# Kernel tuning notes

Hardware: AMD Instinct MI355X
Metric: run time of the kernel (lower is better)

Reference implementation:

```python
import jax, jax.numpy as jnp
import numpy as np

DIM = 1024
HEADS = 16

def setup_inputs() -> dict:
    key = jax.random.key(0)
    k1, k2 = jax.random.split(key)
    x = jax.random.normal(k1, (4, 2048, DIM), dtype=jnp.float32)
    # torch nn.Linear(dim, 3*dim, bias=False): weight shape [3*dim, dim], y = x @ W.T
    W_qkv = jax.random.normal(k2, (3 * DIM, DIM), dtype=jnp.float32) * (DIM ** -0.5)
    return {"x": x, "W_qkv": W_qkv}

def reference(x, W_qkv):
    B, N, D = x.shape
    H = HEADS
    hd = D // H
    scale = hd ** -0.5
    qkv = jnp.einsum('bnd,ed->bne', x, W_qkv)            # [B,N,3D]
    qkv = qkv.reshape(B, N, 3, H, hd).transpose(2, 0, 3, 1, 4)  # [3,B,H,N,hd]
    q, k, v = qkv[0], qkv[1], qkv[2]
    attn = jnp.einsum('bhnd,bhmd->bhnm', q, k) * scale   # [B,H,N,N]
    attn = jax.nn.softmax(attn, axis=-1)                 # dropout is identity at eval
    out = jnp.einsum('bhnm,bhmd->bhnd', attn, v)         # [B,H,N,hd]
    return out.transpose(0, 2, 1, 3).reshape(B, N, D)
```

## Files before the change

kernel.cpp:

```cpp
#include <hip/hip_runtime.h>

typedef unsigned short ushort_t;
typedef short bf16x8 __attribute__((ext_vector_type(8)));
typedef float f32x4 __attribute__((ext_vector_type(4)));
typedef float f32x16 __attribute__((ext_vector_type(16)));

__device__ __forceinline__ unsigned f2bf(float f) {
  union { float f; unsigned u; } v; v.f = f;
  return (v.u + 0x7FFFu + ((v.u >> 16) & 1u)) >> 16;
}

__device__ __forceinline__ void gll16(const void* g, const void* l) {
  __builtin_amdgcn_global_load_lds(
      (const __attribute__((address_space(1))) void*)g,
      (__attribute__((address_space(3))) void*)l, 16, 0, 0);
}

__global__ __launch_bounds__(256) void cvt_both(const float* __restrict__ x,
                                                const float* __restrict__ W,
                                                ushort_t* __restrict__ xb,
                                                ushort_t* __restrict__ wb) {
  int bid = blockIdx.x;
  const float* src;
  ushort_t* dst;
  int i;
  if (bid < 8192) { src = x; dst = xb; i = bid * 256 + threadIdx.x; }
  else            { src = W; dst = wb; i = (bid - 8192) * 256 + threadIdx.x; }
  float4 v = ((const float4*)src)[i];
  uint2 o;
  o.x = f2bf(v.x) | (f2bf(v.y) << 16);
  o.y = f2bf(v.z) | (f2bf(v.w) << 16);
  ((uint2*)dst)[i] = o;
}

__global__ __launch_bounds__(256) void gemm_qkv(const ushort_t* __restrict__ A,
                                                const ushort_t* __restrict__ Bw,
                                                ushort_t* __restrict__ qk,
                                                ushort_t* __restrict__ VT) {
  __shared__ ushort_t As[128 * 64];
  __shared__ ushort_t Bs[128 * 64];
  const int tid = threadIdx.x;
  const int w = tid >> 6, ln = tid & 63;
  const int g = ln >> 4, lr = ln & 15;
  const int bx = blockIdx.x;
  const int swz = (bx & 7) * 192 + (bx >> 3);
  const int nt = swz % 24, mt = swz / 24;
  const int m0 = mt * 128, n0 = nt * 128;
  const int wr = w >> 1, wc = w & 1;
  const float cscale = (nt < 8) ? 0.18033688f : 1.0f;

  f32x4 acc[4][4] = {};

  for (int kt = 0; kt < 16; ++kt) {
#pragma unroll
    for (int q = 0; q < 4; ++q) {
      int chunk = w * 256 + q * 64 + ln;
      int r = chunk >> 3, c = chunk & 7;
      int cs = c ^ (r & 7);
      gll16(A + (size_t)(m0 + r) * 1024 + kt * 64 + cs * 8, As + chunk * 8);
      gll16(Bw + (size_t)(n0 + r) * 1024 + kt * 64 + cs * 8, Bs + chunk * 8);
    }
    __syncthreads();
#pragma unroll
    for (int ks = 0; ks < 2; ++ks) {
      bf16x8 af[4], bfr[4];
#pragma unroll
      for (int mi = 0; mi < 4; ++mi) {
        int row = wr * 64 + mi * 16 + lr;
        af[mi] = *(const bf16x8*)((const char*)As + row * 128 +
                                  ((g * 16 + ks * 64) ^ ((row & 7) << 4)));
      }
#pragma unroll
      for (int ni = 0; ni < 4; ++ni) {
        int row = wc * 64 + ni * 16 + lr;
        bfr[ni] = *(const bf16x8*)((const char*)Bs + row * 128 +
                                   ((g * 16 + ks * 64) ^ ((row & 7) << 4)));
      }
#pragma unroll
      for (int mi = 0; mi < 4; ++mi)
#pragma unroll
        for (int ni = 0; ni < 4; ++ni)
          acc[mi][ni] = __builtin_amdgcn_mfma_f32_16x16x32_bf16(af[mi], bfr[ni],
                                                                acc[mi][ni], 0, 0, 0);
    }
    __syncthreads();
  }

  if (nt < 16) {
#pragma unroll
    for (int mi = 0; mi < 4; ++mi)
#pragma unroll
      for (int ni = 0; ni < 4; ++ni)
#pragma unroll
        for (int r = 0; r < 4; ++r) {
          int row = m0 + wr * 64 + mi * 16 + g * 4 + r;
          int col = n0 + wc * 64 + ni * 16 + lr;
          qk[(size_t)row * 2048 + col] = (ushort_t)f2bf(acc[mi][ni][r] * cscale);
        }
  } else {
    const int b = m0 >> 11;
    const int gp = ((g & 1) << 1) | (g >> 1);
#pragma unroll
    for (int mi = 0; mi < 4; ++mi) {
      int nbase = (m0 & 2047) + wr * 64 + mi * 16 + gp * 4;
#pragma unroll
      for (int ni = 0; ni < 4; ++ni) {
        int f = n0 - 2048 + wc * 64 + ni * 16 + lr;
        int hh = f >> 6, d = f & 63;
        uint2 o;
        o.x = f2bf(acc[mi][ni][0]) | (f2bf(acc[mi][ni][1]) << 16);
        o.y = f2bf(acc[mi][ni][2]) | (f2bf(acc[mi][ni][3]) << 16);
        *(uint2*)(VT + ((size_t)(b * 16 + hh) * 64 + d) * 2048 + nbase) = o;
      }
    }
  }
}

__global__ __launch_bounds__(512) void attn2(const ushort_t* __restrict__ qk,
                                             const ushort_t* __restrict__ VT,
                                             float* __restrict__ out) {
  __shared__ ushort_t Ks[3][2048];
  __shared__ ushort_t Vs[3][2048];
  const int blk = blockIdx.x;
  const int bh = blk & 63, qt = blk >> 6;
  const int b = bh >> 4, hh = bh & 15;
  const int tid = threadIdx.x;
  const int w = tid >> 6, l = tid & 63;
  const int q = l & 31, h = l >> 5;
  const int q0 = qt * 256 + w * 32;
  const int qsw = q & 7;

  const ushort_t* qrow = qk + (size_t)(b * 2048 + q0 + q) * 2048 + hh * 64 + 8 * h;
  bf16x8 qf[4];
#pragma unroll
  for (int m = 0; m < 4; ++m) qf[m] = *(const bf16x8*)(qrow + 16 * m);

  const int st = tid & 255;
  const int rS = st >> 3, cS = st & 7;
  const int cL = cS ^ (rS & 7);
  const bool isK = tid < 256;
  const ushort_t* gsrc =
      isK ? qk + (size_t)(b * 2048 + rS) * 2048 + 1024 + hh * 64 + cL * 8
          : VT + (size_t)(bh * 64 + rS + 32 * (cL >> 2)) * 2048 + (cL & 3) * 8;
  const size_t gstep = isK ? (size_t)32 * 2048 : (size_t)32;
  ushort_t* lbase = isK ? &Ks[0][0] : &Vs[0][0];

  f32x16 oacc0, oacc1;
#pragma unroll
  for (int i = 0; i < 16; ++i) { oacc0[i] = 0.f; oacc1[i] = 0.f; }
  float l_run = 0.f;

  gll16(gsrc, lbase + st * 8);
  gll16(gsrc + gstep, lbase + 2048 + st * 8);
  asm volatile("s_waitcnt vmcnt(1)" ::: "memory");
  __builtin_amdgcn_s_barrier();

  int cur = 0;
  for (int t = 0; t < 64; ++t) {
    int tn = t + 2; if (tn > 63) tn = 63;
    int bufn = cur + 2; if (bufn >= 3) bufn -= 3;
    gll16(gsrc + (size_t)tn * gstep, lbase + bufn * 2048 + st * 8);

    const ushort_t* KsB = Ks[cur];
    const ushort_t* VsB = Vs[cur];

    f32x16 S;
#pragma unroll
    for (int i = 0; i < 16; ++i) S[i] = 0.f;
    __builtin_amdgcn_s_setprio(1);
#pragma unroll
    for (int m = 0; m < 4; ++m) {
      bf16x8 kf = *(const bf16x8*)(KsB + q * 64 + (((2 * m + h) ^ qsw) * 8));
      S = __builtin_amdgcn_mfma_f32_32x32x16_bf16(kf, qf[m], S, 0, 0, 0);
    }
    __builtin_amdgcn_s_setprio(0);

    float p[16];
#pragma unroll
    for (int i = 0; i < 16; ++i) p[i] = __builtin_amdgcn_exp2f(S[i]);
    float s0 = (p[0] + p[1]) + (p[2] + p[3]);
    float s1 = (p[4] + p[5]) + (p[6] + p[7]);
    float s2 = (p[8] + p[9]) + (p[10] + p[11]);
    float s3 = (p[12] + p[13]) + (p[14] + p[15]);
    float ls = (s0 + s1) + (s2 + s3);
    ls += __shfl_xor(ls, 32, 64);
    l_run += ls;

    union { unsigned u[4]; bf16x8 v; } pf0, pf1;
#pragma unroll
    for (int i = 0; i < 4; ++i)
      asm("v_cvt_pk_bf16_f32 %0, %1, %2"
          : "=v"(pf0.u[i]) : "v"(p[2 * i]), "v"(p[2 * i + 1]));
#pragma unroll
    for (int i = 0; i < 4; ++i)
      asm("v_cvt_pk_bf16_f32 %0, %1, %2"
          : "=v"(pf1.u[i]) : "v"(p[8 + 2 * i]), "v"(p[8 + 2 * i + 1]));

    bf16x8 vf0 = *(const bf16x8*)(VsB + q * 64 + (((0 + h) ^ qsw) * 8));
    bf16x8 vf1 = *(const bf16x8*)(VsB + q * 64 + (((2 + h) ^ qsw) * 8));
    bf16x8 vf2 = *(const bf16x8*)(VsB + q * 64 + (((4 + h) ^ qsw) * 8));
    bf16x8 vf3 = *(const bf16x8*)(VsB + q * 64 + (((6 + h) ^ qsw) * 8));

    __builtin_amdgcn_s_setprio(1);
    oacc0 = __builtin_amdgcn_mfma_f32_32x32x16_bf16(vf0, pf0.v, oacc0, 0, 0, 0);
    oacc0 = __builtin_amdgcn_mfma_f32_32x32x16_bf16(vf1, pf1.v, oacc0, 0, 0, 0);
    oacc1 = __builtin_amdgcn_mfma_f32_32x32x16_bf16(vf2, pf0.v, oacc1, 0, 0, 0);
    oacc1 = __builtin_amdgcn_mfma_f32_32x32x16_bf16(vf3, pf1.v, oacc1, 0, 0, 0);
    __builtin_amdgcn_s_setprio(0);

    asm volatile("s_waitcnt vmcnt(1)" ::: "memory");
    __builtin_amdgcn_s_barrier();
    cur += 1; if (cur == 3) cur = 0;
  }

  float inv = 1.0f / l_run;
  float* orow = out + (size_t)(b * 2048 + q0 + q) * 1024 + hh * 64 + 4 * h;
#pragma unroll
  for (int rq = 0; rq < 4; ++rq) {
    float4 o0, o1;
    o0.x = oacc0[rq * 4 + 0] * inv; o0.y = oacc0[rq * 4 + 1] * inv;
    o0.z = oacc0[rq * 4 + 2] * inv; o0.w = oacc0[rq * 4 + 3] * inv;
    o1.x = oacc1[rq * 4 + 0] * inv; o1.y = oacc1[rq * 4 + 1] * inv;
    o1.z = oacc1[rq * 4 + 2] * inv; o1.w = oacc1[rq * 4 + 3] * inv;
    *(float4*)(orow + 8 * rq) = o0;
    *(float4*)(orow + 32 + 8 * rq) = o1;
  }
}

extern "C" void kernel_launch(void* const* d_in, const int* in_sizes, int n_in,
                              void* d_out, int out_size, void* d_ws, size_t ws_size,
                              hipStream_t stream) {
  const float* x = (const float*)d_in[0];
  const float* Wq = (const float*)d_in[1];
  float* out = (float*)d_out;
  char* ws = (char*)d_ws;

  ushort_t* xb = (ushort_t*)ws;
  ushort_t* wb = (ushort_t*)(ws + 16777216);
  ushort_t* qk = (ushort_t*)(ws + 23068672);
  ushort_t* VT = (ushort_t*)(ws + 23068672 + 33554432);

  cvt_both<<<8192 + 3072, 256, 0, stream>>>(x, Wq, xb, wb);
  gemm_qkv<<<64 * 24, 256, 0, stream>>>(xb, wb, qk, VT);
  attn2<<<64 * 8, 512, 0, stream>>>(qk, VT, out);
}
```

Measured before the change: 162.4 us.

## Double-buffer LDS tiles in QKV GEMM to prefetch next K-slice

```diff
diff --git a/kernel.cpp b/kernel.cpp
--- a/kernel.cpp
+++ b/kernel.cpp
@@ -37,8 +37,8 @@
                                                 const ushort_t* __restrict__ Bw,
                                                 ushort_t* __restrict__ qk,
                                                 ushort_t* __restrict__ VT) {
-  __shared__ ushort_t As[128 * 64];
-  __shared__ ushort_t Bs[128 * 64];
+  __shared__ ushort_t As[2][128 * 64];
+  __shared__ ushort_t Bs[2][128 * 64];
   const int tid = threadIdx.x;
   const int w = tid >> 6, ln = tid & 63;
   const int g = ln >> 4, lr = ln & 15;
@@ -49,31 +49,49 @@
   const int wr = w >> 1, wc = w & 1;
   const float cscale = (nt < 8) ? 0.18033688f : 1.0f;
 
+  const int chunkR[4] = { (w * 256 + 0 * 64 + ln) >> 3, (w * 256 + 1 * 64 + ln) >> 3,
+                          (w * 256 + 2 * 64 + ln) >> 3, (w * 256 + 3 * 64 + ln) >> 3 };
+  const int chunkC[4] = { (w * 256 + 0 * 64 + ln) & 7, (w * 256 + 1 * 64 + ln) & 7,
+                          (w * 256 + 2 * 64 + ln) & 7, (w * 256 + 3 * 64 + ln) & 7 };
+
   f32x4 acc[4][4] = {};
 
+#pragma unroll
+  for (int q = 0; q < 4; ++q) {
+    int chunk = w * 256 + q * 64 + ln;
+    int r = chunkR[q], cs = chunkC[q] ^ (r & 7);
+    gll16(A + (size_t)(m0 + r) * 1024 + cs * 8, As[0] + chunk * 8);
+    gll16(Bw + (size_t)(n0 + r) * 1024 + cs * 8, Bs[0] + chunk * 8);
+  }
+  __syncthreads();
+
+  int cur = 0;
   for (int kt = 0; kt < 16; ++kt) {
-#pragma unroll
-    for (int q = 0; q < 4; ++q) {
-      int chunk = w * 256 + q * 64 + ln;
-      int r = chunk >> 3, c = chunk & 7;
-      int cs = c ^ (r & 7);
-      gll16(A + (size_t)(m0 + r) * 1024 + kt * 64 + cs * 8, As + chunk * 8);
-      gll16(Bw + (size_t)(n0 + r) * 1024 + kt * 64 + cs * 8, Bs + chunk * 8);
-    }
-    __syncthreads();
+    if (kt < 15) {
+#pragma unroll
+      for (int q = 0; q < 4; ++q) {
+        int chunk = w * 256 + q * 64 + ln;
+        int r = chunkR[q], cs = chunkC[q] ^ (r & 7);
+        gll16(A + (size_t)(m0 + r) * 1024 + (kt + 1) * 64 + cs * 8,
+              As[cur ^ 1] + chunk * 8);
+        gll16(Bw + (size_t)(n0 + r) * 1024 + (kt + 1) * 64 + cs * 8,
+              Bs[cur ^ 1] + chunk * 8);
+      }
+    }
+
 #pragma unroll
     for (int ks = 0; ks < 2; ++ks) {
       bf16x8 af[4], bfr[4];
 #pragma unroll
       for (int mi = 0; mi < 4; ++mi) {
         int row = wr * 64 + mi * 16 + lr;
-        af[mi] = *(const bf16x8*)((const char*)As + row * 128 +
+        af[mi] = *(const bf16x8*)((const char*)As[cur] + row * 128 +
                                   ((g * 16 + ks * 64) ^ ((row & 7) << 4)));
       }
 #pragma unroll
       for (int ni = 0; ni < 4; ++ni) {
         int row = wc * 64 + ni * 16 + lr;
-        bfr[ni] = *(const bf16x8*)((const char*)Bs + row * 128 +
+        bfr[ni] = *(const bf16x8*)((const char*)Bs[cur] + row * 128 +
                                    ((g * 16 + ks * 64) ^ ((row & 7) << 4)));
       }
 #pragma unroll
@@ -83,7 +101,9 @@
           acc[mi][ni] = __builtin_amdgcn_mfma_f32_16x16x32_bf16(af[mi], bfr[ni],
                                                                 acc[mi][ni], 0, 0, 0);
     }
+
     __syncthreads();
+    cur ^= 1;
   }
 
   if (nt < 16) {
```

Result: slower. 174.9 us (+7.7%).
